# Kernel tuning notes

Hardware: AMD Instinct MI355X
Metric: run time of the kernel (lower is better)

Reference implementation:

```python
import jax, jax.numpy as jnp
import numpy as np
import math

D = 1024
H = 16
DH = D // H
B, M, N = 4, 1024, 2048
LN_EPS = 1e-5


def setup_inputs() -> dict:
    key = jax.random.key(0)
    ks = jax.random.split(key, 8)
    s = 1.0 / math.sqrt(D)  # keep logits well-scaled
    return {
        "Q": jax.random.normal(ks[0], (B, M, D), jnp.float32),
        "KV": jax.random.normal(ks[1], (B, N, D), jnp.float32),
        "log_gate_bias": jax.random.normal(ks[2], (B, N), jnp.float32),
        "Wq": jax.random.normal(ks[3], (D, D), jnp.float32) * s,
        "bq": jnp.zeros((D,), jnp.float32),
        "Wk": jax.random.normal(ks[4], (D, D), jnp.float32) * s,
        "bk": jnp.zeros((D,), jnp.float32),
        "Wv": jax.random.normal(ks[5], (D, D), jnp.float32) * s,
        "bv": jnp.zeros((D,), jnp.float32),
        "Wo": jax.random.normal(ks[6], (D, D), jnp.float32) * s,
        "bo": jnp.zeros((D,), jnp.float32),
        "gamma": jnp.ones((D,), jnp.float32),
        "beta": jnp.zeros((D,), jnp.float32),
    }


def reference(Q, KV, log_gate_bias, Wq, bq, Wk, bk, Wv, bv, Wo, bo, gamma, beta):
    b, m, d = Q.shape
    n = KV.shape[1]
    # projections (torch Linear: x @ W.T + b), split heads -> (b, h, len, dh)
    q = (Q @ Wq.T + bq).reshape(b, m, H, DH).transpose(0, 2, 1, 3)
    k = (KV @ Wk.T + bk).reshape(b, n, H, DH).transpose(0, 2, 1, 3)
    v = (KV @ Wv.T + bv).reshape(b, n, H, DH).transpose(0, 2, 1, 3)
    scores = jnp.einsum('bhmd,bhnd->bhmn', q, k) / math.sqrt(DH)
    # additive gate bias broadcast over heads and queries: (b,1,1,n)
    scores = scores + log_gate_bias[:, None, None, :]
    attn = jax.nn.softmax(scores, axis=-1)
    out = jnp.einsum('bhmn,bhnd->bhmd', attn, v)
    out = out.transpose(0, 2, 1, 3).reshape(b, m, d)
    out = out @ Wo.T + bo
    # dropout p=0.0 (eval) -> identity; residual + LayerNorm
    x = Q + out
    mu = jnp.mean(x, axis=-1, keepdims=True)
    var = jnp.mean(jnp.square(x - mu), axis=-1, keepdims=True)
    return gamma * (x - mu) * jax.lax.rsqrt(var + LN_EPS) + beta
```

## Files before the change

### kernel.cpp

```cpp
#include <hip/hip_runtime.h>
#include <hip/hip_bf16.h>

#define DMODEL 1024
#define NHEAD  16
#define DHEAD  64
#define BB     4
#define MM     1024
#define NN     2048
#define LOG2E  1.4426950408889634f

typedef __attribute__((ext_vector_type(8))) short bf16x8;
typedef __attribute__((ext_vector_type(4))) float f32x4;

#define AS1 __attribute__((address_space(1)))
#define AS3 __attribute__((address_space(3)))

__device__ __forceinline__ unsigned short f2bf(float f) {
  unsigned int u = __builtin_bit_cast(unsigned int, f);
  unsigned int r = (u + 0x7fffu + ((u >> 16) & 1u)) >> 16;
  return (unsigned short)r;
}

__global__ __launch_bounds__(256)
void cast_all(const float* __restrict__ Q, const float* __restrict__ KV,
              const float* __restrict__ W0, const float* __restrict__ W1,
              const float* __restrict__ W2, const float* __restrict__ W3,
              unsigned short* __restrict__ oQ, unsigned short* __restrict__ oKV,
              unsigned short* __restrict__ o0, unsigned short* __restrict__ o1,
              unsigned short* __restrict__ o2, unsigned short* __restrict__ o3)
{
  const int bid = blockIdx.x;
  const float* s; unsigned short* d; int i;
  if (bid < 4096)       { s = Q;  d = oQ;  i = bid * 256 + threadIdx.x; }
  else if (bid < 12288) { s = KV; d = oKV; i = (bid - 4096) * 256 + threadIdx.x; }
  else {
    const int w = (bid - 12288) >> 10;
    s = w == 0 ? W0 : w == 1 ? W1 : w == 2 ? W2 : W3;
    d = w == 0 ? o0 : w == 1 ? o1 : w == 2 ? o2 : o3;
    i = ((bid - 12288) & 1023) * 256 + threadIdx.x;
  }
  const float4 v = ((const float4*)s)[i];
  union { unsigned short us[4]; unsigned long long u64; } o;
  o.us[0] = f2bf(v.x); o.us[1] = f2bf(v.y); o.us[2] = f2bf(v.z); o.us[3] = f2bf(v.w);
  *(unsigned long long*)(d + (size_t)i * 4) = o.u64;
}

__global__ __launch_bounds__(256)
void qkv_gemm(const unsigned short* __restrict__ Qbf,
              const unsigned short* __restrict__ KVbf,
              const unsigned short* __restrict__ Wqb,
              const unsigned short* __restrict__ Wkb,
              const unsigned short* __restrict__ Wvb,
              const float* __restrict__ bq, const float* __restrict__ bk,
              const float* __restrict__ bv,
              unsigned short* __restrict__ qout,
              unsigned short* __restrict__ kout,
              unsigned short* __restrict__ vtout)
{
  __shared__ unsigned short As[2][128 * 32];
  __shared__ unsigned short Ws[2][128 * 32];

  const int bid = blockIdx.x;
  const unsigned short* A; const unsigned short* W; const float* bias;
  int mode, lb, nmb;
  if (bid < 256)      { A = Qbf;  W = Wqb; bias = bq; mode = 0; lb = bid;       nmb = 4; }
  else if (bid < 768) { A = KVbf; W = Wkb; bias = bk; mode = 1; lb = bid - 256; nmb = 8; }
  else                { A = KVbf; W = Wvb; bias = bv; mode = 2; lb = bid - 768; nmb = 8; }
  const int xcd = lb & 7;
  const int l   = lb >> 3;
  const int mb  = xcd * nmb + (l >> 3);
  const int nb  = l & 7;

  const int tid  = threadIdx.x;
  const int wave = tid >> 6;
  const int lane = tid & 63;
  const int l15  = lane & 15;
  const int l4   = lane >> 4;
  const int wm   = wave >> 1;
  const int wn   = wave & 1;
  const size_t row0 = (size_t)mb * 128;
  const size_t col0 = (size_t)nb * 128;

  f32x4 acc[4][4] = {};

  auto stage = [&](int buf, int kt) {
    const unsigned short* Ab = A + row0 * DMODEL + kt * 32;
    const unsigned short* Wb = W + col0 * DMODEL + kt * 32;
#pragma unroll
    for (int is = 0; is < 2; ++is) {
      int cc  = (wave * 2 + is) * 64 + lane;
      int r   = cc >> 2;
      int ch  = cc & 3;
      int sch = ch ^ (r & 3);
      __builtin_amdgcn_global_load_lds(
          (const AS1 void*)(Ab + (size_t)r * DMODEL + sch * 8),
          (AS3 void*)(&As[buf][cc * 8]), 16, 0, 0);
      __builtin_amdgcn_global_load_lds(
          (const AS1 void*)(Wb + (size_t)r * DMODEL + sch * 8),
          (AS3 void*)(&Ws[buf][cc * 8]), 16, 0, 0);
    }
  };

  stage(0, 0);
  __syncthreads();

  for (int kt = 0; kt < 32; ++kt) {
    const int cur = kt & 1;
    if (kt < 31) stage(cur ^ 1, kt + 1);

    bf16x8 af[4], bfr[4];
#pragma unroll
    for (int mi = 0; mi < 4; ++mi) {
      int r = wm * 64 + mi * 16 + l15;
      af[mi] = *(const bf16x8*)&As[cur][r * 32 + ((l4 ^ (r & 3)) << 3)];
    }
#pragma unroll
    for (int ni = 0; ni < 4; ++ni) {
      int r = wn * 64 + ni * 16 + l15;
      bfr[ni] = *(const bf16x8*)&Ws[cur][r * 32 + ((l4 ^ (r & 3)) << 3)];
    }
#pragma unroll
    for (int mi = 0; mi < 4; ++mi)
#pragma unroll
      for (int ni = 0; ni < 4; ++ni)
        acc[mi][ni] = __builtin_amdgcn_mfma_f32_16x16x32_bf16(af[mi], bfr[ni], acc[mi][ni], 0, 0, 0);

    __syncthreads();
  }

#pragma unroll
  for (int mi = 0; mi < 4; ++mi) {
#pragma unroll
    for (int ni = 0; ni < 4; ++ni) {
      const int col = (int)col0 + wn * 64 + ni * 16 + l15;
      const float bcol = bias[col];
      if (mode == 2) {
        const int row = (int)row0 + wm * 64 + mi * 16 + l4 * 4;
        const int b = row >> 11, n = row & 2047;
        const int h = col >> 6, d = col & 63;
        union { unsigned short us[4]; uint2 u; } pk;
#pragma unroll
        for (int i = 0; i < 4; ++i)
          pk.us[i] = __builtin_bit_cast(unsigned short, __float2bfloat16(acc[mi][ni][i] + bcol));
        *(uint2*)(vtout + (((size_t)(b * 16 + h) * 64 + d) << 11) + n) = pk.u;
      } else {
#pragma unroll
        for (int i = 0; i < 4; ++i) {
          const size_t row = row0 + wm * 64 + mi * 16 + l4 * 4 + i;
          float v = acc[mi][ni][i] + bcol;
          if (mode == 0) v *= (0.125f * LOG2E);
          (mode == 0 ? qout : kout)[row * DMODEL + col] =
            __builtin_bit_cast(unsigned short, __float2bfloat16(v));
        }
      }
    }
  }
}

__global__ __launch_bounds__(256)
void gemm_o(const unsigned short* __restrict__ A,
            const unsigned short* __restrict__ W,
            const float* __restrict__ bias,
            const float* __restrict__ resid,
            float* __restrict__ out)
{
  __shared__ unsigned short As[2][64 * 32];
  __shared__ unsigned short Ws[2][128 * 32];

  const int bid = blockIdx.x;
  const int xcd = bid & 7;
  const int l   = bid >> 3;
  const int mb  = xcd * 8 + (l >> 3);
  const int nb  = l & 7;

  const int tid  = threadIdx.x;
  const int wave = tid >> 6;
  const int lane = tid & 63;
  const int l15  = lane & 15;
  const int l4   = lane >> 4;
  const int wm   = wave >> 1;
  const int wn   = wave & 1;
  const size_t row0 = (size_t)mb * 64;
  const size_t col0 = (size_t)nb * 128;

  f32x4 acc[2][4] = {};

  auto stage = [&](int buf, int kt) {
    const unsigned short* Ab = A + row0 * DMODEL + kt * 32;
    const unsigned short* Wb = W + col0 * DMODEL + kt * 32;
    {
      int cc  = tid;
      int r   = cc >> 2;
      int ch  = cc & 3;
      int sch = ch ^ (r & 3);
      __builtin_amdgcn_global_load_lds(
          (const AS1 void*)(Ab + (size_t)r * DMODEL + sch * 8),
          (AS3 void*)(&As[buf][cc * 8]), 16, 0, 0);
    }
#pragma unroll
    for (int is = 0; is < 2; ++is) {
      int cc  = (wave * 2 + is) * 64 + lane;
      int r   = cc >> 2;
      int ch  = cc & 3;
      int sch = ch ^ (r & 3);
      __builtin_amdgcn_global_load_lds(
          (const AS1 void*)(Wb + (size_t)r * DMODEL + sch * 8),
          (AS3 void*)(&Ws[buf][cc * 8]), 16, 0, 0);
    }
  };

  stage(0, 0);
  __syncthreads();

  for (int kt = 0; kt < 32; ++kt) {
    const int cur = kt & 1;
    if (kt < 31) stage(cur ^ 1, kt + 1);

    bf16x8 af[2], bfr[4];
#pragma unroll
    for (int mi = 0; mi < 2; ++mi) {
      int r = wm * 32 + mi * 16 + l15;
      af[mi] = *(const bf16x8*)&As[cur][r * 32 + ((l4 ^ (r & 3)) << 3)];
    }
#pragma unroll
    for (int ni = 0; ni < 4; ++ni) {
      int r = wn * 64 + ni * 16 + l15;
      bfr[ni] = *(const bf16x8*)&Ws[cur][r * 32 + ((l4 ^ (r & 3)) << 3)];
    }
#pragma unroll
    for (int mi = 0; mi < 2; ++mi)
#pragma unroll
      for (int ni = 0; ni < 4; ++ni)
        acc[mi][ni] = __builtin_amdgcn_mfma_f32_16x16x32_bf16(af[mi], bfr[ni], acc[mi][ni], 0, 0, 0);

    __syncthreads();
  }

#pragma unroll
  for (int mi = 0; mi < 2; ++mi) {
#pragma unroll
    for (int ni = 0; ni < 4; ++ni) {
      const int col = (int)col0 + wn * 64 + ni * 16 + l15;
      const float bcol = bias[col];
#pragma unroll
      for (int i = 0; i < 4; ++i) {
        const size_t row = row0 + wm * 32 + mi * 16 + l4 * 4 + i;
        const size_t idx = row * DMODEL + col;
        out[idx] = resid[idx] + acc[mi][ni][i] + bcol;
      }
    }
  }
}

__global__ __launch_bounds__(256, 4)
void attn_kernel(const unsigned short* __restrict__ qb,
                 const unsigned short* __restrict__ kb,
                 const unsigned short* __restrict__ vt,
                 const float* __restrict__ lgb,
                 unsigned short* __restrict__ attn)
{
  __shared__ unsigned short Ks[2][64 * 64];
  __shared__ unsigned short Vs[2][64 * 64];
  __shared__ unsigned short Ps[4][16 * 64];

  const int tid  = threadIdx.x;
  const int wave = tid >> 6;
  const int lane = tid & 63;
  const int l15  = lane & 15;
  const int l4   = lane >> 4;

  const int bid  = blockIdx.x;
  const int xcd  = bid & 7;
  const int slot = bid >> 3;
  const int m_i  = slot & 15;
  const int grp  = slot >> 4;
  const int bh   = grp * 8 + xcd;
  const int b    = bh >> 4;
  const int h    = bh & 15;
  const int m0   = m_i * 64;

  const unsigned short* qg = qb + ((size_t)(b * MM + m0)) * DMODEL + h * DHEAD;
  const unsigned short* kg = kb + ((size_t)b * NN) * DMODEL + h * DHEAD;
  const unsigned short* vg = vt + ((size_t)(b * NHEAD + h)) * (DHEAD * (size_t)NN);
  const float* gg = lgb + (size_t)b * NN;

  bf16x8 qf0, qf1;
  {
    const unsigned short* qrow = qg + (size_t)(wave * 16 + l15) * DMODEL;
    qf0 = *(const bf16x8*)(qrow + l4 * 8);
    qf1 = *(const bf16x8*)(qrow + 32 + l4 * 8);
  }

  bf16x8 ones;
  {
    const short one = (l15 == 0) ? (short)0x3f80 : (short)0;
#pragma unroll
    for (int j = 0; j < 8; ++j) ones[j] = one;
  }

  auto stageKV = [&](int buf, int nt) {
    const int n0 = nt * 64;
#pragma unroll
    for (int is = 0; is < 2; ++is) {
      int cc = (wave * 2 + is) * 64 + lane;
      int r  = cc >> 3;
      int ch = cc & 7;
      __builtin_amdgcn_global_load_lds(
          (const AS1 void*)(kg + (size_t)(n0 + r) * DMODEL + ((ch ^ (r & 7)) << 3)),
          (AS3 void*)(&Ks[buf][cc * 8]), 16, 0, 0);
    }
#pragma unroll
    for (int is = 0; is < 2; ++is) {
      int cc = (wave * 2 + is) * 64 + lane;
      int r  = cc >> 3;
      int ch = cc & 7;
      __builtin_amdgcn_global_load_lds(
          (const AS1 void*)(vg + (size_t)r * NN + n0 + ((ch ^ (r & 7)) << 3)),
          (AS3 void*)(&Vs[buf][cc * 8]), 16, 0, 0);
    }
  };

  f32x4 gc[4], gn[4];
#pragma unroll
  for (int ni = 0; ni < 4; ++ni)
    gc[ni] = *(const f32x4*)&gg[ni * 16 + l4 * 4];

  stageKV(0, 0);

  f32x4 ovec[5] = {};
  float mrow = -1e30f;
  unsigned short* Pw = &Ps[wave][0];
  const int pbase = l15 * 128;
  const int s7 = l15 & 7;

  for (int nt = 0; nt < NN / 64; ++nt) {
    const int cur = nt & 1;
    asm volatile("s_waitcnt vmcnt(0)" ::: "memory");
    __builtin_amdgcn_s_barrier();
    __builtin_amdgcn_sched_barrier(0);
    if (nt < NN / 64 - 1) {
      stageKV(cur ^ 1, nt + 1);
#pragma unroll
      for (int ni = 0; ni < 4; ++ni)
        gn[ni] = *(const f32x4*)&gg[(nt + 1) * 64 + ni * 16 + l4 * 4];
    }

    f32x4 s[4];
    __builtin_amdgcn_s_setprio(1);
#pragma unroll
    for (int ni = 0; ni < 4; ++ni) {
      const int r = ni * 16 + l15;
      const int c0 = l4 ^ (r & 7);
      bf16x8 kf0 = *(const bf16x8*)&Ks[cur][r * 64 + (c0 << 3)];
      bf16x8 kf1 = *(const bf16x8*)&Ks[cur][r * 64 + ((c0 ^ 4) << 3)];
      f32x4 z = {};
      z = __builtin_amdgcn_mfma_f32_16x16x32_bf16(kf0, qf0, z, 0, 0, 0);
      s[ni] = __builtin_amdgcn_mfma_f32_16x16x32_bf16(kf1, qf1, z, 0, 0, 0);
    }
    __builtin_amdgcn_s_setprio(0);

    float tmax = -1e30f;
#pragma unroll
    for (int ni = 0; ni < 4; ++ni) {
#pragma unroll
      for (int i = 0; i < 4; ++i)
        s[ni][i] = fmaf(gc[ni][i], LOG2E, s[ni][i]);
      tmax = fmaxf(tmax, fmaxf(fmaxf(s[ni][0], s[ni][1]), fmaxf(s[ni][2], s[ni][3])));
    }
    tmax = fmaxf(tmax, __shfl_xor(tmax, 16));
    tmax = fmaxf(tmax, __shfl_xor(tmax, 32));

    if (!__all(tmax <= mrow)) {
      const float mnew  = fmaxf(mrow, tmax);
      const float alpha = __builtin_amdgcn_exp2f(mrow - mnew);
      mrow = mnew;
      const int abase = l4 << 2;
#pragma unroll
      for (int i = 0; i < 4; ++i) {
        const float ai = __shfl(alpha, abase + i);
        ovec[0][i] *= ai; ovec[1][i] *= ai; ovec[2][i] *= ai;
        ovec[3][i] *= ai; ovec[4][i] *= ai;
      }
    }

#pragma unroll
    for (int ni = 0; ni < 4; ++ni) {
      union { unsigned short us[4]; uint2 u; } pk;
#pragma unroll
      for (int i = 0; i < 4; ++i)
        pk.us[i] = __builtin_bit_cast(unsigned short,
                     __float2bfloat16(__builtin_amdgcn_exp2f(s[ni][i] - mrow)));
      *(uint2*)((char*)Pw + pbase + (((ni * 4 + l4) ^ (s7 << 1)) << 3)) = pk.u;
    }
    asm volatile("s_waitcnt lgkmcnt(0)" ::: "memory");
    __builtin_amdgcn_sched_barrier(0);

    __builtin_amdgcn_s_setprio(1);
#pragma unroll
    for (int ks2 = 0; ks2 < 2; ++ks2) {
      const bf16x8 pf = *(const bf16x8*)((const char*)Pw + pbase + (((ks2 * 4 + l4) ^ s7) << 4));
#pragma unroll
      for (int di = 0; di < 4; ++di) {
        const int d = di * 16 + l15;
        const bf16x8 vf = *(const bf16x8*)&Vs[cur][d * 64 + (((ks2 * 4 + l4) ^ (d & 7)) << 3)];
        ovec[di] = __builtin_amdgcn_mfma_f32_16x16x32_bf16(pf, vf, ovec[di], 0, 0, 0);
      }
      ovec[4] = __builtin_amdgcn_mfma_f32_16x16x32_bf16(pf, ones, ovec[4], 0, 0, 0);
    }
    __builtin_amdgcn_s_setprio(0);

    if (nt < NN / 64 - 1) {
#pragma unroll
      for (int ni = 0; ni < 4; ++ni) gc[ni] = gn[ni];
    }
  }

  const int lsrc = lane & 48;
  float linv[4];
#pragma unroll
  for (int i = 0; i < 4; ++i)
    linv[i] = 1.0f / __shfl(ovec[4][i], lsrc);
#pragma unroll
  for (int di = 0; di < 4; ++di)
#pragma unroll
    for (int i = 0; i < 4; ++i) {
      const int row = m0 + wave * 16 + l4 * 4 + i;
      const int col = h * DHEAD + di * 16 + l15;
      attn[((size_t)(b * MM + row)) * DMODEL + col] =
        __builtin_bit_cast(unsigned short, __float2bfloat16(ovec[di][i] * linv[i]));
    }
}

__global__ __launch_bounds__(256)
void ln_kernel(const float* __restrict__ x, const float* __restrict__ gamma,
               const float* __restrict__ beta, float* __restrict__ out)
{
  __shared__ float sh1[4], sh2[4];
  const int t = threadIdx.x;
  const size_t row = blockIdx.x;
  const float4 v = ((const float4*)(x + row * DMODEL))[t];

  float s = v.x + v.y + v.z + v.w;
#pragma unroll
  for (int m = 1; m < 64; m <<= 1) s += __shfl_xor(s, m);
  if ((t & 63) == 0) sh1[t >> 6] = s;
  __syncthreads();
  const float mu = (sh1[0] + sh1[1] + sh1[2] + sh1[3]) * (1.0f / DMODEL);

  const float dx = v.x - mu, dy = v.y - mu, dz = v.z - mu, dw = v.w - mu;
  float q = dx * dx + dy * dy + dz * dz + dw * dw;
#pragma unroll
  for (int m = 1; m < 64; m <<= 1) q += __shfl_xor(q, m);
  if ((t & 63) == 0) sh2[t >> 6] = q;
  __syncthreads();
  const float var = (sh2[0] + sh2[1] + sh2[2] + sh2[3]) * (1.0f / DMODEL);
  const float rstd = rsqrtf(var + 1e-5f);

  const float4 g  = ((const float4*)gamma)[t];
  const float4 be = ((const float4*)beta)[t];
  float4 o;
  o.x = dx * rstd * g.x + be.x;
  o.y = dy * rstd * g.y + be.y;
  o.z = dz * rstd * g.z + be.z;
  o.w = dw * rstd * g.w + be.w;
  ((float4*)(out + row * DMODEL))[t] = o;
}

extern "C" void kernel_launch(void* const* d_in, const int* in_sizes, int n_in,
                              void* d_out, int out_size, void* d_ws, size_t ws_size,
                              hipStream_t stream)
{
  const float* Qf    = (const float*)d_in[0];
  const float* KVf   = (const float*)d_in[1];
  const float* lgb   = (const float*)d_in[2];
  const float* Wq    = (const float*)d_in[3];
  const float* bq    = (const float*)d_in[4];
  const float* Wk    = (const float*)d_in[5];
  const float* bk    = (const float*)d_in[6];
  const float* Wv    = (const float*)d_in[7];
  const float* bv    = (const float*)d_in[8];
  const float* Wo    = (const float*)d_in[9];
  const float* bo    = (const float*)d_in[10];
  const float* gamma = (const float*)d_in[11];
  const float* beta  = (const float*)d_in[12];
  float* out = (float*)d_out;

  char* ws = (char*)d_ws;
  unsigned short* Qbf   = (unsigned short*)(ws + 0);
  unsigned short* attnb = Qbf;
  unsigned short* KVbf  = (unsigned short*)(ws + 8388608);
  float*          xbuf  = (float*)(ws + 8388608);
  unsigned short* Wqb = (unsigned short*)(ws + 25165824);
  unsigned short* Wkb = (unsigned short*)(ws + 27262976);
  unsigned short* Wvb = (unsigned short*)(ws + 29360128);
  unsigned short* Wob = (unsigned short*)(ws + 31457280);
  unsigned short* qbuf  = (unsigned short*)(ws + 33554432);
  unsigned short* kbuf  = (unsigned short*)(ws + 41943040);
  unsigned short* vtbuf = (unsigned short*)(ws + 58720256);

  dim3 blk(256);
  cast_all<<<16384, blk, 0, stream>>>(Qf, KVf, Wq, Wk, Wv, Wo,
                                      Qbf, KVbf, Wqb, Wkb, Wvb, Wob);

  qkv_gemm<<<1280, blk, 0, stream>>>(Qbf, KVbf, Wqb, Wkb, Wvb,
                                     bq, bk, bv, qbuf, kbuf, vtbuf);

  attn_kernel<<<1024, blk, 0, stream>>>(qbuf, kbuf, vtbuf, lgb, attnb);

  gemm_o<<<512, blk, 0, stream>>>(attnb, Wob, bo, Qf, xbuf);

  ln_kernel<<<4096, blk, 0, stream>>>(xbuf, gamma, beta, out);
}
```

Baseline: 179.0 us.

## Double attention block to 8 waves sharing K/V tiles, stage gate bias via LDS

```diff
diff --git a/kernel.cpp b/kernel.cpp
--- a/kernel.cpp
+++ b/kernel.cpp
@@ -83,30 +83,29 @@
 
   f32x4 acc[4][4] = {};
 
-  auto stage = [&](int buf, int kt) {
-    const unsigned short* Ab = A + row0 * DMODEL + kt * 32;
-    const unsigned short* Wb = W + col0 * DMODEL + kt * 32;
-#pragma unroll
-    for (int is = 0; is < 2; ++is) {
-      int cc  = (wave * 2 + is) * 64 + lane;
-      int r   = cc >> 2;
-      int ch  = cc & 3;
-      int sch = ch ^ (r & 3);
-      __builtin_amdgcn_global_load_lds(
-          (const AS1 void*)(Ab + (size_t)r * DMODEL + sch * 8),
-          (AS3 void*)(&As[buf][cc * 8]), 16, 0, 0);
-      __builtin_amdgcn_global_load_lds(
-          (const AS1 void*)(Wb + (size_t)r * DMODEL + sch * 8),
-          (AS3 void*)(&Ws[buf][cc * 8]), 16, 0, 0);
-    }
+  const int cc0 = (wave * 2) * 64 + lane;
+  const int cc1 = cc0 + 64;
+  const int r0 = cc0 >> 2, sch0 = (cc0 & 3) ^ (r0 & 3);
+  const int r1 = cc1 >> 2, sch1 = (cc1 & 3) ^ (r1 & 3);
+  const unsigned short* ap0 = A + (row0 + r0) * DMODEL + sch0 * 8;
+  const unsigned short* ap1 = A + (row0 + r1) * DMODEL + sch1 * 8;
+  const unsigned short* wp0 = W + (col0 + r0) * DMODEL + sch0 * 8;
+  const unsigned short* wp1 = W + (col0 + r1) * DMODEL + sch1 * 8;
+
+  auto stage = [&](int buf) {
+    __builtin_amdgcn_global_load_lds((const AS1 void*)ap0, (AS3 void*)(&As[buf][cc0 * 8]), 16, 0, 0);
+    __builtin_amdgcn_global_load_lds((const AS1 void*)ap1, (AS3 void*)(&As[buf][cc1 * 8]), 16, 0, 0);
+    __builtin_amdgcn_global_load_lds((const AS1 void*)wp0, (AS3 void*)(&Ws[buf][cc0 * 8]), 16, 0, 0);
+    __builtin_amdgcn_global_load_lds((const AS1 void*)wp1, (AS3 void*)(&Ws[buf][cc1 * 8]), 16, 0, 0);
+    ap0 += 32; ap1 += 32; wp0 += 32; wp1 += 32;
   };
 
-  stage(0, 0);
+  stage(0);
   __syncthreads();
 
   for (int kt = 0; kt < 32; ++kt) {
     const int cur = kt & 1;
-    if (kt < 31) stage(cur ^ 1, kt + 1);
+    if (kt < 31) stage(cur ^ 1);
 
     bf16x8 af[4], bfr[4];
 #pragma unroll
@@ -185,36 +184,28 @@
 
   f32x4 acc[2][4] = {};
 
-  auto stage = [&](int buf, int kt) {
-    const unsigned short* Ab = A + row0 * DMODEL + kt * 32;
-    const unsigned short* Wb = W + col0 * DMODEL + kt * 32;
-    {
-      int cc  = tid;
-      int r   = cc >> 2;
-      int ch  = cc & 3;
-      int sch = ch ^ (r & 3);
-      __builtin_amdgcn_global_load_lds(
-          (const AS1 void*)(Ab + (size_t)r * DMODEL + sch * 8),
-          (AS3 void*)(&As[buf][cc * 8]), 16, 0, 0);
-    }
-#pragma unroll
-    for (int is = 0; is < 2; ++is) {
-      int cc  = (wave * 2 + is) * 64 + lane;
-      int r   = cc >> 2;
-      int ch  = cc & 3;
-      int sch = ch ^ (r & 3);
-      __builtin_amdgcn_global_load_lds(
-          (const AS1 void*)(Wb + (size_t)r * DMODEL + sch * 8),
-          (AS3 void*)(&Ws[buf][cc * 8]), 16, 0, 0);
-    }
+  const int ra = tid >> 2, scha = (tid & 3) ^ (ra & 3);
+  const int cc0 = (wave * 2) * 64 + lane;
+  const int cc1 = cc0 + 64;
+  const int r0 = cc0 >> 2, sch0 = (cc0 & 3) ^ (r0 & 3);
+  const int r1 = cc1 >> 2, sch1 = (cc1 & 3) ^ (r1 & 3);
+  const unsigned short* ap  = A + (row0 + ra) * DMODEL + scha * 8;
+  const unsigned short* wp0 = W + (col0 + r0) * DMODEL + sch0 * 8;
+  const unsigned short* wp1 = W + (col0 + r1) * DMODEL + sch1 * 8;
+
+  auto stage = [&](int buf) {
+    __builtin_amdgcn_global_load_lds((const AS1 void*)ap,  (AS3 void*)(&As[buf][tid * 8]), 16, 0, 0);
+    __builtin_amdgcn_global_load_lds((const AS1 void*)wp0, (AS3 void*)(&Ws[buf][cc0 * 8]), 16, 0, 0);
+    __builtin_amdgcn_global_load_lds((const AS1 void*)wp1, (AS3 void*)(&Ws[buf][cc1 * 8]), 16, 0, 0);
+    ap += 32; wp0 += 32; wp1 += 32;
   };
 
-  stage(0, 0);
+  stage(0);
   __syncthreads();
 
   for (int kt = 0; kt < 32; ++kt) {
     const int cur = kt & 1;
-    if (kt < 31) stage(cur ^ 1, kt + 1);
+    if (kt < 31) stage(cur ^ 1);
 
     bf16x8 af[2], bfr[4];
 #pragma unroll
@@ -252,7 +243,7 @@
   }
 }
 
-__global__ __launch_bounds__(256, 4)
+__global__ __launch_bounds__(512, 4)
 void attn_kernel(const unsigned short* __restrict__ qb,
                  const unsigned short* __restrict__ kb,
                  const unsigned short* __restrict__ vt,
@@ -261,7 +252,8 @@
 {
   __shared__ unsigned short Ks[2][64 * 64];
   __shared__ unsigned short Vs[2][64 * 64];
-  __shared__ unsigned short Ps[4][16 * 64];
+  __shared__ float Gs[2][64];
+  __shared__ unsigned short Ps[8][16 * 64];
 
   const int tid  = threadIdx.x;
   const int wave = tid >> 6;
@@ -272,17 +264,16 @@
   const int bid  = blockIdx.x;
   const int xcd  = bid & 7;
   const int slot = bid >> 3;
-  const int m_i  = slot & 15;
-  const int grp  = slot >> 4;
+  const int m_i  = slot & 7;
+  const int grp  = slot >> 3;
   const int bh   = grp * 8 + xcd;
   const int b    = bh >> 4;
   const int h    = bh & 15;
-  const int m0   = m_i * 64;
+  const int m0   = m_i * 128;
 
   const unsigned short* qg = qb + ((size_t)(b * MM + m0)) * DMODEL + h * DHEAD;
   const unsigned short* kg = kb + ((size_t)b * NN) * DMODEL + h * DHEAD;
   const unsigned short* vg = vt + ((size_t)(b * NHEAD + h)) * (DHEAD * (size_t)NN);
-  const float* gg = lgb + (size_t)b * NN;
 
   bf16x8 qf0, qf1;
   {
@@ -298,34 +289,21 @@
     for (int j = 0; j < 8; ++j) ones[j] = one;
   }
 
-  auto stageKV = [&](int buf, int nt) {
-    const int n0 = nt * 64;
-#pragma unroll
-    for (int is = 0; is < 2; ++is) {
-      int cc = (wave * 2 + is) * 64 + lane;
-      int r  = cc >> 3;
-      int ch = cc & 7;
-      __builtin_amdgcn_global_load_lds(
-          (const AS1 void*)(kg + (size_t)(n0 + r) * DMODEL + ((ch ^ (r & 7)) << 3)),
-          (AS3 void*)(&Ks[buf][cc * 8]), 16, 0, 0);
-    }
-#pragma unroll
-    for (int is = 0; is < 2; ++is) {
-      int cc = (wave * 2 + is) * 64 + lane;
-      int r  = cc >> 3;
-      int ch = cc & 7;
-      __builtin_amdgcn_global_load_lds(
-          (const AS1 void*)(vg + (size_t)r * NN + n0 + ((ch ^ (r & 7)) << 3)),
-          (AS3 void*)(&Vs[buf][cc * 8]), 16, 0, 0);
-    }
+  const int sr = tid >> 3;
+  const int sc = (tid & 7) ^ (sr & 7);
+  const unsigned short* kp = kg + (size_t)sr * DMODEL + (sc << 3);
+  const unsigned short* vp = vg + (size_t)sr * NN + (sc << 3);
+  const float* gp = lgb + (size_t)b * NN + lane;
+
+  auto stage = [&](int buf) {
+    if (wave == 0)
+      __builtin_amdgcn_global_load_lds((const AS1 void*)gp, (AS3 void*)(&Gs[buf][lane]), 4, 0, 0);
+    __builtin_amdgcn_global_load_lds((const AS1 void*)kp, (AS3 void*)(&Ks[buf][tid * 8]), 16, 0, 0);
+    __builtin_amdgcn_global_load_lds((const AS1 void*)vp, (AS3 void*)(&Vs[buf][tid * 8]), 16, 0, 0);
+    kp += 64 * DMODEL; vp += 64; gp += 64;
   };
 
-  f32x4 gc[4], gn[4];
-#pragma unroll
-  for (int ni = 0; ni < 4; ++ni)
-    gc[ni] = *(const f32x4*)&gg[ni * 16 + l4 * 4];
-
-  stageKV(0, 0);
+  stage(0);
 
   f32x4 ovec[5] = {};
   float mrow = -1e30f;
@@ -336,14 +314,10 @@
   for (int nt = 0; nt < NN / 64; ++nt) {
     const int cur = nt & 1;
     asm volatile("s_waitcnt vmcnt(0)" ::: "memory");
+    __builtin_amdgcn_sched_barrier(0);
     __builtin_amdgcn_s_barrier();
     __builtin_amdgcn_sched_barrier(0);
-    if (nt < NN / 64 - 1) {
-      stageKV(cur ^ 1, nt + 1);
-#pragma unroll
-      for (int ni = 0; ni < 4; ++ni)
-        gn[ni] = *(const f32x4*)&gg[(nt + 1) * 64 + ni * 16 + l4 * 4];
-    }
+    if (nt < NN / 64 - 1) stage(cur ^ 1);
 
     f32x4 s[4];
     __builtin_amdgcn_s_setprio(1);
@@ -362,9 +336,11 @@
     float tmax = -1e30f;
 #pragma unroll
     for (int ni = 0; ni < 4; ++ni) {
-#pragma unroll
-      for (int i = 0; i < 4; ++i)
-        s[ni][i] = fmaf(gc[ni][i], LOG2E, s[ni][i]);
+      const float4 g = *(const float4*)&Gs[cur][ni * 16 + l4 * 4];
+      s[ni][0] = fmaf(g.x, LOG2E, s[ni][0]);
+      s[ni][1] = fmaf(g.y, LOG2E, s[ni][1]);
+      s[ni][2] = fmaf(g.z, LOG2E, s[ni][2]);
+      s[ni][3] = fmaf(g.w, LOG2E, s[ni][3]);
       tmax = fmaxf(tmax, fmaxf(fmaxf(s[ni][0], s[ni][1]), fmaxf(s[ni][2], s[ni][3])));
     }
     tmax = fmaxf(tmax, __shfl_xor(tmax, 16));
@@ -408,11 +384,6 @@
       ovec[4] = __builtin_amdgcn_mfma_f32_16x16x32_bf16(pf, ones, ovec[4], 0, 0, 0);
     }
     __builtin_amdgcn_s_setprio(0);
-
-    if (nt < NN / 64 - 1) {
-#pragma unroll
-      for (int ni = 0; ni < 4; ++ni) gc[ni] = gn[ni];
-    }
   }
 
   const int lsrc = lane & 48;
@@ -498,16 +469,15 @@
   unsigned short* kbuf  = (unsigned short*)(ws + 41943040);
   unsigned short* vtbuf = (unsigned short*)(ws + 58720256);
 
-  dim3 blk(256);
-  cast_all<<<16384, blk, 0, stream>>>(Qf, KVf, Wq, Wk, Wv, Wo,
-                                      Qbf, KVbf, Wqb, Wkb, Wvb, Wob);
-
-  qkv_gemm<<<1280, blk, 0, stream>>>(Qbf, KVbf, Wqb, Wkb, Wvb,
-                                     bq, bk, bv, qbuf, kbuf, vtbuf);
-
-  attn_kernel<<<1024, blk, 0, stream>>>(qbuf, kbuf, vtbuf, lgb, attnb);
-
-  gemm_o<<<512, blk, 0, stream>>>(attnb, Wob, bo, Qf, xbuf);
-
-  ln_kernel<<<4096, blk, 0, stream>>>(xbuf, gamma, beta, out);
-}
+  cast_all<<<16384, dim3(256), 0, stream>>>(Qf, KVf, Wq, Wk, Wv, Wo,
+                                            Qbf, KVbf, Wqb, Wkb, Wvb, Wob);
+
+  qkv_gemm<<<1280, dim3(256), 0, stream>>>(Qbf, KVbf, Wqb, Wkb, Wvb,
+                                           bq, bk, bv, qbuf, kbuf, vtbuf);
+
+  attn_kernel<<<512, dim3(512), 0, stream>>>(qbuf, kbuf, vtbuf, lgb, attnb);
+
+  gemm_o<<<512, dim3(256), 0, stream>>>(attnb, Wob, bo, Qf, xbuf);
+
+  ln_kernel<<<4096, dim3(256), 0, stream>>>(xbuf, gamma, beta, out);
+}
```

Measured after the change: 171.5 us. 4.2% less time.
